# Performance work log

Measured on AMD Instinct MI355X. Metric: run time of the kernel, lower is better.

Reference implementation:

```python
import jax, jax.numpy as jnp
import numpy as np

N, T, V = 256, 70, 64
B, H, C = 6, 1024, 4  # n_blocks, n_internal_units, n_class
SPECTRAL_RADIUS = 0.99
INPUT_SCALING = 0.2


def setup_inputs() -> dict:
    key = jax.random.key(0)
    k1, k2, k3, k4 = jax.random.split(key, 4)
    X = jax.random.normal(k1, (N, T, V), dtype=jnp.float32)
    # spectral-radius-normalized reservoir weights (circular law: rho(G/sqrt(H)) ~ 1)
    W_res = jax.random.normal(k2, (B, H, H), dtype=jnp.float32) * (SPECTRAL_RADIUS / jnp.sqrt(H).astype(jnp.float32))
    # +/-1 Bernoulli input weights scaled by input_scaling
    W_in = jnp.sign(jax.random.normal(k3, (B, H, V), dtype=jnp.float32)) * INPUT_SCALING
    W_lin = jax.random.normal(k4, (T, C, B * H), dtype=jnp.float32) * 0.02
    b_lin = jnp.zeros((T, C), dtype=jnp.float32)
    return {"X": X, "W_res": W_res, "W_in": W_in, "W_lin": W_lin, "b_lin": b_lin}


def reference(X, W_res, W_in, W_lin, b_lin):
    # Echo state recurrence: s_t = tanh(W_res @ s_{t-1} + W_in @ x_t), per block
    # (leak=None, noise_level=0.0, n_drop=0 as in module defaults)
    n, t_len, v = X.shape
    b, h, _ = W_res.shape

    def step(s, x_t):  # s: [B,N,H], x_t: [N,V]
        pre = jnp.einsum('bij,bnj->bni', W_res, s) + jnp.einsum('bhv,nv->bnh', W_in, x_t)
        s_new = jnp.tanh(pre)
        return s_new, s_new

    s0 = jnp.zeros((b, n, h), dtype=X.dtype)
    _, states = jax.lax.scan(step, s0, jnp.swapaxes(X, 0, 1))  # [T,B,N,H]

    # per-timestep features: concat blocks -> [T,N,B*H]
    feats = jnp.transpose(states, (0, 2, 1, 3)).reshape(t_len, n, b * h)
    # per-timestep linear heads
    logits = jnp.einsum('tnf,tcf->tnc', feats, W_lin) + b_lin[:, None, :]  # [T,N,C]
    preds = jnp.argmax(logits, axis=-1)  # [T,N], matches forward()'s class_dict
    return logits, preds
```

## Files before the change

kernel.cpp:

```cpp
#include <hip/hip_runtime.h>
#include <stdint.h>


typedef _Float16 f16;
typedef _Float16 f16x8 __attribute__((ext_vector_type(8)));
typedef float floatx4 __attribute__((ext_vector_type(4)));

#define N_TOT 256
#define T_TOT 70
#define V_TOT 64
#define B_TOT 6
#define H_TOT 1024
#define C_TOT 4
#define F_TOT (B_TOT * H_TOT)
#define G_TOT 192
#define LDA 72
#define LO_SCALE 4096.0f
#define LO_INV   (1.0f / 4096.0f)

union H8 { f16 h[8]; uint4 v; };

__global__ __launch_bounds__(256)
void split_f32(const float* __restrict__ src, f16* __restrict__ hi,
               f16* __restrict__ lo, int n)
{
    const int i = (blockIdx.x * 256 + threadIdx.x) * 8;
    if (i + 8 > n) return;
    const float4 a = *(const float4*)&src[i];
    const float4 b = *(const float4*)&src[i + 4];
    const float x[8] = {a.x, a.y, a.z, a.w, b.x, b.y, b.z, b.w};
    H8 H, L;
#pragma unroll
    for (int j = 0; j < 8; ++j) {
        const f16 h = (f16)x[j];
        H.h[j] = h;
        L.h[j] = (f16)((x[j] - (float)h) * LO_SCALE);
    }
    *(uint4*)&hi[i] = H.v;
    *(uint4*)&lo[i] = L.v;
}

__global__ __launch_bounds__(256)
void head_reduce(const float* __restrict__ part,
                 const float* __restrict__ b_lin,
                 float* __restrict__ logits,
                 float* __restrict__ preds)
{
    const int t = blockIdx.x;
    const int n = threadIdx.x;

    float a0 = b_lin[t * C_TOT + 0];
    float a1 = b_lin[t * C_TOT + 1];
    float a2 = b_lin[t * C_TOT + 2];
    float a3 = b_lin[t * C_TOT + 3];

    const float* p = part + (((size_t)t * G_TOT) * N_TOT + n) * C_TOT;
    for (int g = 0; g < G_TOT; ++g) {
        const float4 v = *(const float4*)&p[(size_t)g * N_TOT * C_TOT];
        a0 += v.x; a1 += v.y; a2 += v.z; a3 += v.w;
    }

    float4 o = {a0, a1, a2, a3};
    *(float4*)&logits[((size_t)t * N_TOT + n) * C_TOT] = o;

    int arg = 0;
    float best = a0;
    if (a1 > best) { best = a1; arg = 1; }
    if (a2 > best) { best = a2; arg = 2; }
    if (a3 > best) { best = a3; arg = 3; }
    preds[(size_t)t * N_TOT + n] = (float)arg;
}

__global__ __launch_bounds__(256)
void esn_step_fused(const f16* __restrict__ Xhi,   const f16* __restrict__ Xlo,
                    const f16* __restrict__ Whi,   const f16* __restrict__ Wlo,
                    const f16* __restrict__ Wihi,  const f16* __restrict__ Wilo,
                    const f16* __restrict__ shi_p, const f16* __restrict__ slo_p,
                    f16* __restrict__ shi_n,       f16* __restrict__ slo_n,
                    const float* __restrict__ W_lin, float* __restrict__ part,
                    int t, int first)
{
    __shared__ f16 As_hi[64 * LDA];
    __shared__ f16 As_lo[64 * LDA];
    __shared__ f16 Bs_hi[32 * LDA];
    __shared__ f16 Bs_lo[32 * LDA];

    const int id  = blockIdx.x;
    const int b   = id >> 7;
    const int rem = id & 127;
    const int mt  = rem >> 5;
    const int it  = rem & 31;

    const int tid  = threadIdx.x;
    const int wm   = tid >> 6;
    const int lane = tid & 63;
    const int l16  = lane & 15;
    const int oct  = lane >> 4;

    const int ra = tid >> 2;
    const int ca = (tid & 3) << 4;
    const int rb = tid >> 3;
    const int cb = (tid & 7) << 3;

    floatx4 acc[2], accl[2];
#pragma unroll
    for (int j = 0; j < 2; ++j) { acc[j] = (floatx4)(0.0f); accl[j] = (floatx4)(0.0f); }

    if (!first) {
        const f16* Ah = shi_p + (size_t)(b * N_TOT + mt * 64 + ra) * H_TOT + ca;
        const f16* Al = slo_p + (size_t)(b * N_TOT + mt * 64 + ra) * H_TOT + ca;
        const f16* Bh = Whi   + (size_t)(b * H_TOT + it * 32 + rb) * H_TOT + cb;
        const f16* Bl = Wlo   + (size_t)(b * H_TOT + it * 32 + rb) * H_TOT + cb;

        uint4 pah0, pah1, pal0, pal1, pbh, pbl;
#define LOAD_CHUNK(J0)                                   \
        do {                                             \
            pah0 = *(const uint4*)&Ah[(J0) + 0];         \
            pah1 = *(const uint4*)&Ah[(J0) + 8];         \
            pal0 = *(const uint4*)&Al[(J0) + 0];         \
            pal1 = *(const uint4*)&Al[(J0) + 8];         \
            pbh  = *(const uint4*)&Bh[(J0)];             \
            pbl  = *(const uint4*)&Bl[(J0)];             \
        } while (0)

        LOAD_CHUNK(0);
        for (int kc = 0; kc < 16; ++kc) {
            if (kc) __syncthreads();
            *(uint4*)&As_hi[ra * LDA + ca]     = pah0;
            *(uint4*)&As_hi[ra * LDA + ca + 8] = pah1;
            *(uint4*)&As_lo[ra * LDA + ca]     = pal0;
            *(uint4*)&As_lo[ra * LDA + ca + 8] = pal1;
            *(uint4*)&Bs_hi[rb * LDA + cb]     = pbh;
            *(uint4*)&Bs_lo[rb * LDA + cb]     = pbl;
            __syncthreads();
            if (kc < 15) LOAD_CHUNK((kc + 1) * 64);

#pragma unroll
            for (int kk = 0; kk < 64; kk += 32) {
                const int ar = (wm * 16 + l16) * LDA + kk + oct * 8;
                const f16x8 ah = *(const f16x8*)&As_hi[ar];
                const f16x8 al = *(const f16x8*)&As_lo[ar];
#pragma unroll
                for (int nf = 0; nf < 2; ++nf) {
                    const int br = (nf * 16 + l16) * LDA + kk + oct * 8;
                    const f16x8 bh = *(const f16x8*)&Bs_hi[br];
                    const f16x8 bl = *(const f16x8*)&Bs_lo[br];
                    acc[nf]  = __builtin_amdgcn_mfma_f32_16x16x32_f16(ah, bh, acc[nf], 0, 0, 0);
                    accl[nf] = __builtin_amdgcn_mfma_f32_16x16x32_f16(ah, bl, accl[nf], 0, 0, 0);
                    accl[nf] = __builtin_amdgcn_mfma_f32_16x16x32_f16(al, bh, accl[nf], 0, 0, 0);
                }
            }
        }
#undef LOAD_CHUNK
        __syncthreads();
    }

    {
        const size_t xb = ((size_t)(mt * 64 + ra) * T_TOT + t) * V_TOT + ca;
        *(uint4*)&As_hi[ra * LDA + ca]     = *(const uint4*)&Xhi[xb];
        *(uint4*)&As_hi[ra * LDA + ca + 8] = *(const uint4*)&Xhi[xb + 8];
        *(uint4*)&As_lo[ra * LDA + ca]     = *(const uint4*)&Xlo[xb];
        *(uint4*)&As_lo[ra * LDA + ca + 8] = *(const uint4*)&Xlo[xb + 8];
        const size_t wb = (size_t)(b * H_TOT + it * 32 + rb) * V_TOT + cb;
        *(uint4*)&Bs_hi[rb * LDA + cb] = *(const uint4*)&Wihi[wb];
        *(uint4*)&Bs_lo[rb * LDA + cb] = *(const uint4*)&Wilo[wb];
        __syncthreads();
#pragma unroll
        for (int kk = 0; kk < 64; kk += 32) {
            const int ar = (wm * 16 + l16) * LDA + kk + oct * 8;
            const f16x8 ah = *(const f16x8*)&As_hi[ar];
            const f16x8 al = *(const f16x8*)&As_lo[ar];
#pragma unroll
            for (int nf = 0; nf < 2; ++nf) {
                const int br = (nf * 16 + l16) * LDA + kk + oct * 8;
                const f16x8 bh = *(const f16x8*)&Bs_hi[br];
                const f16x8 bl = *(const f16x8*)&Bs_lo[br];
                acc[nf]  = __builtin_amdgcn_mfma_f32_16x16x32_f16(ah, bh, acc[nf], 0, 0, 0);
                accl[nf] = __builtin_amdgcn_mfma_f32_16x16x32_f16(ah, bl, accl[nf], 0, 0, 0);
                accl[nf] = __builtin_amdgcn_mfma_f32_16x16x32_f16(al, bh, accl[nf], 0, 0, 0);
            }
        }
    }

    const int nbase = mt * 64;
    const int ibase = it * 32;

    const float* wl = W_lin + (size_t)t * C_TOT * F_TOT + b * H_TOT + ibase;
    float w[4][2];
#pragma unroll
    for (int c = 0; c < 4; ++c)
#pragma unroll
        for (int nf = 0; nf < 2; ++nf)
            w[c][nf] = wl[(size_t)c * F_TOT + nf * 16 + l16];

    float sval[2][4];
#pragma unroll
    for (int nf = 0; nf < 2; ++nf)
#pragma unroll
        for (int r = 0; r < 4; ++r) {
            const int m  = wm * 16 + oct * 4 + r;
            const int ii = nf * 16 + l16;
            const float s = tanhf(acc[nf][r] + accl[nf][r] * LO_INV);
            sval[nf][r] = s;
            const f16 h = (f16)s;
            const size_t oidx = (size_t)(b * N_TOT + nbase + m) * H_TOT + ibase + ii;
            shi_n[oidx] = h;
            slo_n[oidx] = (f16)((s - (float)h) * LO_SCALE);
        }

    const int g = b * 32 + it;
#pragma unroll
    for (int r = 0; r < 4; ++r) {
        float v[4];
#pragma unroll
        for (int c = 0; c < 4; ++c) {
            float x = sval[0][r] * w[c][0] + sval[1][r] * w[c][1];
            x += __shfl_xor(x, 1);
            x += __shfl_xor(x, 2);
            x += __shfl_xor(x, 4);
            x += __shfl_xor(x, 8);
            v[c] = x;
        }
        if (l16 == 0) {
            const int n = nbase + wm * 16 + oct * 4 + r;
            float4 o = {v[0], v[1], v[2], v[3]};
            *(float4*)&part[(((size_t)t * G_TOT + g) * N_TOT + n) * C_TOT] = o;
        }
    }
}

extern "C" void kernel_launch(void* const* d_in, const int* in_sizes, int n_in,
                              void* d_out, int out_size, void* d_ws, size_t ws_size,
                              hipStream_t stream) {
    const float* X     = (const float*)d_in[0];
    const float* W_res = (const float*)d_in[1];
    const float* W_in  = (const float*)d_in[2];
    const float* W_lin = (const float*)d_in[3];
    const float* b_lin = (const float*)d_in[4];

    float* out    = (float*)d_out;
    float* logits = out;
    float* preds  = out + (size_t)T_TOT * N_TOT * C_TOT;

    const size_t nWres = (size_t)B_TOT * H_TOT * H_TOT;
    const size_t nWin  = (size_t)B_TOT * H_TOT * V_TOT;
    const size_t nX    = (size_t)N_TOT * T_TOT * V_TOT;
    const size_t nS    = (size_t)B_TOT * N_TOT * H_TOT;
    const size_t nPart = (size_t)T_TOT * G_TOT * N_TOT * C_TOT;

    f16* p    = (f16*)d_ws;
    f16* Whi  = p;  p += nWres;
    f16* Wlo  = p;  p += nWres;
    f16* Wihi = p;  p += nWin;
    f16* Wilo = p;  p += nWin;
    f16* Xhi  = p;  p += nX;
    f16* Xlo  = p;  p += nX;
    f16* sAh  = p;  p += nS;
    f16* sAl  = p;  p += nS;
    f16* sBh  = p;  p += nS;
    f16* sBl  = p;  p += nS;
    float* part = (float*)p;

    split_f32<<<(int)(nWres / 2048), 256, 0, stream>>>(W_res, Whi, Wlo, (int)nWres);
    split_f32<<<(int)(nWin  / 2048), 256, 0, stream>>>(W_in, Wihi, Wilo, (int)nWin);
    split_f32<<<(int)(nX    / 2048), 256, 0, stream>>>(X, Xhi, Xlo, (int)nX);

    for (int t = 0; t < T_TOT; ++t) {
        const f16 *ph, *pl;
        f16 *nh, *nl;
        if (t & 1) { ph = sBh; pl = sBl; nh = sAh; nl = sAl; }
        else       { ph = sAh; pl = sAl; nh = sBh; nl = sBl; }
        esn_step_fused<<<B_TOT * 4 * 32, 256, 0, stream>>>(
            Xhi, Xlo, Whi, Wlo, Wihi, Wilo, ph, pl, nh, nl,
            W_lin, part, t, t == 0 ? 1 : 0);
    }
    head_reduce<<<T_TOT, 256, 0, stream>>>(part, b_lin, logits, preds);
}
```

Measured before the change: 1.791 ms.

## Split K across waves with LDS cross-wave reduction in ESN step kernel

Each wave now computes the full 64x32 output tile over a quarter of the K chunks (split-K across the four waves) instead of owning 16 rows over all K. Per-wave partial accumulators are then reduced through a shared-memory buffer that aliases the staging tiles. Launch bounds now request 3 blocks per SM. This reuses each B fragment across four M sub-tiles per wave to cut LDS reads per MFMA. In exchange it quadruples accumulator registers, adds an LDS reduction step with an extra barrier, and leaves three of four waves idle during each chunk's compute phase.

```diff
diff --git a/kernel.cpp b/kernel.cpp
--- a/kernel.cpp
+++ b/kernel.cpp
@@ -71,7 +71,17 @@
     preds[(size_t)t * N_TOT + n] = (float)arg;
 }
 
-__global__ __launch_bounds__(256)
+union SBuf {
+    struct {
+        f16 As_hi[64 * LDA];
+        f16 As_lo[64 * LDA];
+        f16 Bs_hi[32 * LDA];
+        f16 Bs_lo[32 * LDA];
+    } s;
+    float red[12][2][64][4];
+};
+
+__global__ __launch_bounds__(256, 3)
 void esn_step_fused(const f16* __restrict__ Xhi,   const f16* __restrict__ Xlo,
                     const f16* __restrict__ Whi,   const f16* __restrict__ Wlo,
                     const f16* __restrict__ Wihi,  const f16* __restrict__ Wilo,
@@ -80,10 +90,11 @@
                     const float* __restrict__ W_lin, float* __restrict__ part,
                     int t, int first)
 {
-    __shared__ f16 As_hi[64 * LDA];
-    __shared__ f16 As_lo[64 * LDA];
-    __shared__ f16 Bs_hi[32 * LDA];
-    __shared__ f16 Bs_lo[32 * LDA];
+    __shared__ SBuf sb;
+    f16* As_hi = sb.s.As_hi;
+    f16* As_lo = sb.s.As_lo;
+    f16* Bs_hi = sb.s.Bs_hi;
+    f16* Bs_lo = sb.s.Bs_lo;
 
     const int id  = blockIdx.x;
     const int b   = id >> 7;
@@ -92,7 +103,7 @@
     const int it  = rem & 31;
 
     const int tid  = threadIdx.x;
-    const int wm   = tid >> 6;
+    const int wv   = tid >> 6;
     const int lane = tid & 63;
     const int l16  = lane & 15;
     const int oct  = lane >> 4;
@@ -102,9 +113,11 @@
     const int rb = tid >> 3;
     const int cb = (tid & 7) << 3;
 
-    floatx4 acc[2], accl[2];
-#pragma unroll
-    for (int j = 0; j < 2; ++j) { acc[j] = (floatx4)(0.0f); accl[j] = (floatx4)(0.0f); }
+    floatx4 acc[4][2], accl[4][2];
+#pragma unroll
+    for (int m = 0; m < 4; ++m)
+#pragma unroll
+        for (int j = 0; j < 2; ++j) { acc[m][j] = (floatx4)(0.0f); accl[m][j] = (floatx4)(0.0f); }
 
     if (!first) {
         const f16* Ah = shi_p + (size_t)(b * N_TOT + mt * 64 + ra) * H_TOT + ca;
@@ -135,19 +148,28 @@
             __syncthreads();
             if (kc < 15) LOAD_CHUNK((kc + 1) * 64);
 
-#pragma unroll
-            for (int kk = 0; kk < 64; kk += 32) {
-                const int ar = (wm * 16 + l16) * LDA + kk + oct * 8;
-                const f16x8 ah = *(const f16x8*)&As_hi[ar];
-                const f16x8 al = *(const f16x8*)&As_lo[ar];
-#pragma unroll
-                for (int nf = 0; nf < 2; ++nf) {
-                    const int br = (nf * 16 + l16) * LDA + kk + oct * 8;
-                    const f16x8 bh = *(const f16x8*)&Bs_hi[br];
-                    const f16x8 bl = *(const f16x8*)&Bs_lo[br];
-                    acc[nf]  = __builtin_amdgcn_mfma_f32_16x16x32_f16(ah, bh, acc[nf], 0, 0, 0);
-                    accl[nf] = __builtin_amdgcn_mfma_f32_16x16x32_f16(ah, bl, accl[nf], 0, 0, 0);
-                    accl[nf] = __builtin_amdgcn_mfma_f32_16x16x32_f16(al, bh, accl[nf], 0, 0, 0);
+            if ((kc & 3) == wv) {
+#pragma unroll
+                for (int kk = 0; kk < 64; kk += 32) {
+                    f16x8 ah[4], al[4];
+#pragma unroll
+                    for (int m = 0; m < 4; ++m) {
+                        const int ar = (m * 16 + l16) * LDA + kk + oct * 8;
+                        ah[m] = *(const f16x8*)&As_hi[ar];
+                        al[m] = *(const f16x8*)&As_lo[ar];
+                    }
+#pragma unroll
+                    for (int nf = 0; nf < 2; ++nf) {
+                        const int br = (nf * 16 + l16) * LDA + kk + oct * 8;
+                        const f16x8 bh = *(const f16x8*)&Bs_hi[br];
+                        const f16x8 bl = *(const f16x8*)&Bs_lo[br];
+#pragma unroll
+                        for (int m = 0; m < 4; ++m) {
+                            acc[m][nf]  = __builtin_amdgcn_mfma_f32_16x16x32_f16(ah[m], bh, acc[m][nf], 0, 0, 0);
+                            accl[m][nf] = __builtin_amdgcn_mfma_f32_16x16x32_f16(ah[m], bl, accl[m][nf], 0, 0, 0);
+                            accl[m][nf] = __builtin_amdgcn_mfma_f32_16x16x32_f16(al[m], bh, accl[m][nf], 0, 0, 0);
+                        }
+                    }
                 }
             }
         }
@@ -165,21 +187,55 @@
         *(uint4*)&Bs_hi[rb * LDA + cb] = *(const uint4*)&Wihi[wb];
         *(uint4*)&Bs_lo[rb * LDA + cb] = *(const uint4*)&Wilo[wb];
         __syncthreads();
-#pragma unroll
-        for (int kk = 0; kk < 64; kk += 32) {
-            const int ar = (wm * 16 + l16) * LDA + kk + oct * 8;
-            const f16x8 ah = *(const f16x8*)&As_hi[ar];
-            const f16x8 al = *(const f16x8*)&As_lo[ar];
+
+        if (wv < 2) {
+            const int kk = wv * 32;
+            f16x8 ah[4], al[4];
+#pragma unroll
+            for (int m = 0; m < 4; ++m) {
+                const int ar = (m * 16 + l16) * LDA + kk + oct * 8;
+                ah[m] = *(const f16x8*)&As_hi[ar];
+                al[m] = *(const f16x8*)&As_lo[ar];
+            }
 #pragma unroll
             for (int nf = 0; nf < 2; ++nf) {
                 const int br = (nf * 16 + l16) * LDA + kk + oct * 8;
                 const f16x8 bh = *(const f16x8*)&Bs_hi[br];
                 const f16x8 bl = *(const f16x8*)&Bs_lo[br];
-                acc[nf]  = __builtin_amdgcn_mfma_f32_16x16x32_f16(ah, bh, acc[nf], 0, 0, 0);
-                accl[nf] = __builtin_amdgcn_mfma_f32_16x16x32_f16(ah, bl, accl[nf], 0, 0, 0);
-                accl[nf] = __builtin_amdgcn_mfma_f32_16x16x32_f16(al, bh, accl[nf], 0, 0, 0);
+#pragma unroll
+                for (int m = 0; m < 4; ++m) {
+                    acc[m][nf]  = __builtin_amdgcn_mfma_f32_16x16x32_f16(ah[m], bh, acc[m][nf], 0, 0, 0);
+                    accl[m][nf] = __builtin_amdgcn_mfma_f32_16x16x32_f16(ah[m], bl, accl[m][nf], 0, 0, 0);
+                    accl[m][nf] = __builtin_amdgcn_mfma_f32_16x16x32_f16(al[m], bh, accl[m][nf], 0, 0, 0);
+                }
             }
         }
+        __syncthreads();
+    }
+
+#pragma unroll
+    for (int d = 0; d < 4; ++d) {
+        if (d == wv) continue;
+        const int slot = wv * 3 + (d < wv ? d : d - 1);
+#pragma unroll
+        for (int nf = 0; nf < 2; ++nf) {
+            floatx4 c = acc[d][nf] + accl[d][nf] * LO_INV;
+            *(floatx4*)&sb.red[slot][nf][lane][0] = c;
+        }
+    }
+    __syncthreads();
+
+    floatx4 tot[2];
+#pragma unroll
+    for (int nf = 0; nf < 2; ++nf)
+        tot[nf] = acc[wv][nf] + accl[wv][nf] * LO_INV;
+#pragma unroll
+    for (int w = 0; w < 4; ++w) {
+        if (w == wv) continue;
+        const int slot = w * 3 + (wv < w ? wv : wv - 1);
+#pragma unroll
+        for (int nf = 0; nf < 2; ++nf)
+            tot[nf] += *(const floatx4*)&sb.red[slot][nf][lane][0];
     }
 
     const int nbase = mt * 64;
@@ -198,9 +254,9 @@
     for (int nf = 0; nf < 2; ++nf)
 #pragma unroll
         for (int r = 0; r < 4; ++r) {
-            const int m  = wm * 16 + oct * 4 + r;
+            const int m  = wv * 16 + oct * 4 + r;
             const int ii = nf * 16 + l16;
-            const float s = tanhf(acc[nf][r] + accl[nf][r] * LO_INV);
+            const float s = tanhf(tot[nf][r]);
             sval[nf][r] = s;
             const f16 h = (f16)s;
             const size_t oidx = (size_t)(b * N_TOT + nbase + m) * H_TOT + ibase + ii;
@@ -222,7 +278,7 @@
             v[c] = x;
         }
         if (l16 == 0) {
-            const int n = nbase + wm * 16 + oct * 4 + r;
+            const int n = nbase + wv * 16 + oct * 4 + r;
             float4 o = {v[0], v[1], v[2], v[3]};
             *(float4*)&part[(((size_t)t * G_TOT + g) * N_TOT + n) * C_TOT] = o;
         }
@@ -246,7 +302,6 @@
     const size_t nWin  = (size_t)B_TOT * H_TOT * V_TOT;
     const size_t nX    = (size_t)N_TOT * T_TOT * V_TOT;
     const size_t nS    = (size_t)B_TOT * N_TOT * H_TOT;
-    const size_t nPart = (size_t)T_TOT * G_TOT * N_TOT * C_TOT;
 
     f16* p    = (f16*)d_ws;
     f16* Whi  = p;  p += nWres;
```

After: 2.983 ms. 1.67x slower.

## Load reservoir weight fragments directly into registers, bypassing shared memory

Applied to the files above, without the earlier changes.

The B operand (W_res and W_in hi/lo halves) is now read from global memory straight into MFMA fragment registers instead of being staged through shared memory. The K loop is unrolled by two with double-buffered register fragments, and an occupancy hint of 3 blocks per CU is added to launch bounds. This removes LDS traffic and bank pressure for the weight tiles and shrinks shared memory use. In exchange, register pressure rises and each 4-wave group re-reads the same weight rows from global memory or cache, since all four waves now fetch the B fragments independently.

```diff
diff --git a/kernel.cpp b/kernel.cpp
--- a/kernel.cpp
+++ b/kernel.cpp
@@ -71,7 +71,7 @@
     preds[(size_t)t * N_TOT + n] = (float)arg;
 }
 
-__global__ __launch_bounds__(256)
+__global__ __launch_bounds__(256, 3)
 void esn_step_fused(const f16* __restrict__ Xhi,   const f16* __restrict__ Xlo,
                     const f16* __restrict__ Whi,   const f16* __restrict__ Wlo,
                     const f16* __restrict__ Wihi,  const f16* __restrict__ Wilo,
@@ -82,8 +82,6 @@
 {
     __shared__ f16 As_hi[64 * LDA];
     __shared__ f16 As_lo[64 * LDA];
-    __shared__ f16 Bs_hi[32 * LDA];
-    __shared__ f16 Bs_lo[32 * LDA];
 
     const int id  = blockIdx.x;
     const int b   = id >> 7;
@@ -99,85 +97,119 @@
 
     const int ra = tid >> 2;
     const int ca = (tid & 3) << 4;
-    const int rb = tid >> 3;
-    const int cb = (tid & 7) << 3;
 
     floatx4 acc[2], accl[2];
 #pragma unroll
     for (int j = 0; j < 2; ++j) { acc[j] = (floatx4)(0.0f); accl[j] = (floatx4)(0.0f); }
+
+    const size_t browH[2] = { (size_t)(0 * 16 + l16) * H_TOT,
+                              (size_t)(1 * 16 + l16) * H_TOT };
 
     if (!first) {
         const f16* Ah = shi_p + (size_t)(b * N_TOT + mt * 64 + ra) * H_TOT + ca;
         const f16* Al = slo_p + (size_t)(b * N_TOT + mt * 64 + ra) * H_TOT + ca;
-        const f16* Bh = Whi   + (size_t)(b * H_TOT + it * 32 + rb) * H_TOT + cb;
-        const f16* Bl = Wlo   + (size_t)(b * H_TOT + it * 32 + rb) * H_TOT + cb;
-
-        uint4 pah0, pah1, pal0, pal1, pbh, pbl;
-#define LOAD_CHUNK(J0)                                   \
+        const f16* Wh = Whi + (size_t)(b * H_TOT + it * 32) * H_TOT;
+        const f16* Wl = Wlo + (size_t)(b * H_TOT + it * 32) * H_TOT;
+
+        uint4 pah0, pah1, pal0, pal1;
+        f16x8 bh0[2][2], bl0[2][2], bh1[2][2], bl1[2][2];
+
+#define LOAD_A(J0)                                       \
         do {                                             \
             pah0 = *(const uint4*)&Ah[(J0) + 0];         \
             pah1 = *(const uint4*)&Ah[(J0) + 8];         \
             pal0 = *(const uint4*)&Al[(J0) + 0];         \
             pal1 = *(const uint4*)&Al[(J0) + 8];         \
-            pbh  = *(const uint4*)&Bh[(J0)];             \
-            pbl  = *(const uint4*)&Bl[(J0)];             \
         } while (0)
-
-        LOAD_CHUNK(0);
-        for (int kc = 0; kc < 16; ++kc) {
+#define LOAD_B(J0, BH, BL)                                               \
+        do {                                                             \
+            _Pragma("unroll")                                            \
+            for (int k2 = 0; k2 < 2; ++k2)                               \
+                _Pragma("unroll")                                        \
+                for (int nf = 0; nf < 2; ++nf) {                         \
+                    const size_t o = browH[nf] + (J0) + k2 * 32 + oct * 8; \
+                    BH[k2][nf] = *(const f16x8*)&Wh[o];                  \
+                    BL[k2][nf] = *(const f16x8*)&Wl[o];                  \
+                }                                                        \
+        } while (0)
+#define STORE_A()                                        \
+        do {                                             \
+            *(uint4*)&As_hi[ra * LDA + ca]     = pah0;   \
+            *(uint4*)&As_hi[ra * LDA + ca + 8] = pah1;   \
+            *(uint4*)&As_lo[ra * LDA + ca]     = pal0;   \
+            *(uint4*)&As_lo[ra * LDA + ca + 8] = pal1;   \
+        } while (0)
+#define COMPUTE(BH, BL)                                                        \
+        do {                                                                   \
+            _Pragma("unroll")                                                  \
+            for (int k2 = 0; k2 < 2; ++k2) {                                   \
+                const int ar = (wm * 16 + l16) * LDA + k2 * 32 + oct * 8;      \
+                const f16x8 ah = *(const f16x8*)&As_hi[ar];                    \
+                const f16x8 al = *(const f16x8*)&As_lo[ar];                    \
+                _Pragma("unroll")                                              \
+                for (int nf = 0; nf < 2; ++nf) {                               \
+                    acc[nf]  = __builtin_amdgcn_mfma_f32_16x16x32_f16(ah, BH[k2][nf], acc[nf], 0, 0, 0);  \
+                    accl[nf] = __builtin_amdgcn_mfma_f32_16x16x32_f16(ah, BL[k2][nf], accl[nf], 0, 0, 0); \
+                    accl[nf] = __builtin_amdgcn_mfma_f32_16x16x32_f16(al, BH[k2][nf], accl[nf], 0, 0, 0); \
+                }                                                              \
+            }                                                                  \
+        } while (0)
+
+        LOAD_A(0);
+        LOAD_B(0, bh0, bl0);
+        for (int kc = 0; kc < 16; kc += 2) {
             if (kc) __syncthreads();
-            *(uint4*)&As_hi[ra * LDA + ca]     = pah0;
-            *(uint4*)&As_hi[ra * LDA + ca + 8] = pah1;
-            *(uint4*)&As_lo[ra * LDA + ca]     = pal0;
-            *(uint4*)&As_lo[ra * LDA + ca + 8] = pal1;
-            *(uint4*)&Bs_hi[rb * LDA + cb]     = pbh;
-            *(uint4*)&Bs_lo[rb * LDA + cb]     = pbl;
+            STORE_A();
             __syncthreads();
-            if (kc < 15) LOAD_CHUNK((kc + 1) * 64);
-
-#pragma unroll
-            for (int kk = 0; kk < 64; kk += 32) {
-                const int ar = (wm * 16 + l16) * LDA + kk + oct * 8;
-                const f16x8 ah = *(const f16x8*)&As_hi[ar];
-                const f16x8 al = *(const f16x8*)&As_lo[ar];
-#pragma unroll
-                for (int nf = 0; nf < 2; ++nf) {
-                    const int br = (nf * 16 + l16) * LDA + kk + oct * 8;
-                    const f16x8 bh = *(const f16x8*)&Bs_hi[br];
-                    const f16x8 bl = *(const f16x8*)&Bs_lo[br];
-                    acc[nf]  = __builtin_amdgcn_mfma_f32_16x16x32_f16(ah, bh, acc[nf], 0, 0, 0);
-                    accl[nf] = __builtin_amdgcn_mfma_f32_16x16x32_f16(ah, bl, accl[nf], 0, 0, 0);
-                    accl[nf] = __builtin_amdgcn_mfma_f32_16x16x32_f16(al, bh, accl[nf], 0, 0, 0);
-                }
+            LOAD_A((kc + 1) * 64);
+            LOAD_B((kc + 1) * 64, bh1, bl1);
+            COMPUTE(bh0, bl0);
+            __syncthreads();
+            STORE_A();
+            __syncthreads();
+            if (kc + 2 < 16) {
+                LOAD_A((kc + 2) * 64);
+                LOAD_B((kc + 2) * 64, bh0, bl0);
             }
-        }
-#undef LOAD_CHUNK
+            COMPUTE(bh1, bl1);
+        }
+#undef LOAD_A
+#undef LOAD_B
+#undef STORE_A
+#undef COMPUTE
         __syncthreads();
     }
 
     {
+        const f16* Wih = Wihi + (size_t)(b * H_TOT + it * 32) * V_TOT;
+        const f16* Wil = Wilo + (size_t)(b * H_TOT + it * 32) * V_TOT;
+        f16x8 bh[2][2], bl[2][2];
+#pragma unroll
+        for (int k2 = 0; k2 < 2; ++k2)
+#pragma unroll
+            for (int nf = 0; nf < 2; ++nf) {
+                const size_t o = (size_t)(nf * 16 + l16) * V_TOT + k2 * 32 + oct * 8;
+                bh[k2][nf] = *(const f16x8*)&Wih[o];
+                bl[k2][nf] = *(const f16x8*)&Wil[o];
+            }
+
         const size_t xb = ((size_t)(mt * 64 + ra) * T_TOT + t) * V_TOT + ca;
         *(uint4*)&As_hi[ra * LDA + ca]     = *(const uint4*)&Xhi[xb];
         *(uint4*)&As_hi[ra * LDA + ca + 8] = *(const uint4*)&Xhi[xb + 8];
         *(uint4*)&As_lo[ra * LDA + ca]     = *(const uint4*)&Xlo[xb];
         *(uint4*)&As_lo[ra * LDA + ca + 8] = *(const uint4*)&Xlo[xb + 8];
-        const size_t wb = (size_t)(b * H_TOT + it * 32 + rb) * V_TOT + cb;
-        *(uint4*)&Bs_hi[rb * LDA + cb] = *(const uint4*)&Wihi[wb];
-        *(uint4*)&Bs_lo[rb * LDA + cb] = *(const uint4*)&Wilo[wb];
         __syncthreads();
-#pragma unroll
-        for (int kk = 0; kk < 64; kk += 32) {
-            const int ar = (wm * 16 + l16) * LDA + kk + oct * 8;
+
+#pragma unroll
+        for (int k2 = 0; k2 < 2; ++k2) {
+            const int ar = (wm * 16 + l16) * LDA + k2 * 32 + oct * 8;
             const f16x8 ah = *(const f16x8*)&As_hi[ar];
             const f16x8 al = *(const f16x8*)&As_lo[ar];
 #pragma unroll
             for (int nf = 0; nf < 2; ++nf) {
-                const int br = (nf * 16 + l16) * LDA + kk + oct * 8;
-                const f16x8 bh = *(const f16x8*)&Bs_hi[br];
-                const f16x8 bl = *(const f16x8*)&Bs_lo[br];
-                acc[nf]  = __builtin_amdgcn_mfma_f32_16x16x32_f16(ah, bh, acc[nf], 0, 0, 0);
-                accl[nf] = __builtin_amdgcn_mfma_f32_16x16x32_f16(ah, bl, accl[nf], 0, 0, 0);
-                accl[nf] = __builtin_amdgcn_mfma_f32_16x16x32_f16(al, bh, accl[nf], 0, 0, 0);
+                acc[nf]  = __builtin_amdgcn_mfma_f32_16x16x32_f16(ah, bh[k2][nf], acc[nf], 0, 0, 0);
+                accl[nf] = __builtin_amdgcn_mfma_f32_16x16x32_f16(ah, bl[k2][nf], accl[nf], 0, 0, 0);
+                accl[nf] = __builtin_amdgcn_mfma_f32_16x16x32_f16(al, bh[k2][nf], accl[nf], 0, 0, 0);
             }
         }
     }
@@ -246,7 +278,6 @@
     const size_t nWin  = (size_t)B_TOT * H_TOT * V_TOT;
     const size_t nX    = (size_t)N_TOT * T_TOT * V_TOT;
     const size_t nS    = (size_t)B_TOT * N_TOT * H_TOT;
-    const size_t nPart = (size_t)T_TOT * G_TOT * N_TOT * C_TOT;
 
     f16* p    = (f16*)d_ws;
     f16* Whi  = p;  p += nWres;
```

Measured after the change: 3.892 ms. +117.3%, slower.
